# Optimization experiments

Measured on AMD Instinct MI355X. Metric: run time of the kernel, lower is better.

The kernel has to match this reference:

```python
import jax, jax.numpy as jnp
import numpy as np

POOL_LEN = 128  # agent tokens (AdaptiveAvgPool1d output size)

def setup_inputs() -> dict:
    key = jax.random.key(0)
    ks = jax.random.split(key, 7)
    B, D, L = 8, 512, 4096
    s = 1.0 / np.sqrt(D)
    return {
        "x":  jax.random.normal(ks[0], (B, D, L), dtype=jnp.float32),
        "Wq": jax.random.normal(ks[1], (D, D), dtype=jnp.float32) * s,
        "bq": jax.random.normal(ks[2], (D,), dtype=jnp.float32) * 0.01,
        "Wk": jax.random.normal(ks[3], (D, D), dtype=jnp.float32) * s,
        "bk": jax.random.normal(ks[4], (D,), dtype=jnp.float32) * 0.01,
        "Wv": jax.random.normal(ks[5], (D, D), dtype=jnp.float32) * s,
        "bv": jax.random.normal(ks[6], (D,), dtype=jnp.float32) * 0.01,
    }

def reference(x, Wq, bq, Wk, bk, Wv, bv):
    # x: [B, D, L] channel-first, as in the torch module
    xt = jnp.swapaxes(x, -1, -2)               # [B, L, D]
    q = xt @ Wq.T + bq                         # [B, L, D]
    k = xt @ Wk.T + bk                         # [B, L, D]
    v = xt @ Wv.T + bv                         # [B, L, D]
    B, L, D = q.shape
    # AdaptiveAvgPool1d(L -> POOL_LEN): uniform segment mean since L % POOL_LEN == 0
    a = q.reshape(B, POOL_LEN, L // POOL_LEN, D).mean(axis=2)  # [B, P, D]
    # stage 1: agents attend to keys, aggregate values (no 1/sqrt(d) scaling in original)
    c = jax.nn.softmax(jnp.einsum('bpd,bld->bpl', a, k), axis=-1) @ v  # [B, P, D]
    # stage 2: queries attend to agents
    r = jax.nn.softmax(jnp.einsum('bld,bpd->blp', q, a), axis=-1) @ c  # [B, L, D]
    return jnp.swapaxes(r, -1, -2)             # [B, D, L]
```

## Files before the change

### kernel.cpp

```cpp
#include <hip/hip_runtime.h>
#include <hip/hip_fp16.h>

typedef _Float16 f16;
using frag16 = __attribute__((ext_vector_type(8))) _Float16;
using f32x4  = __attribute__((ext_vector_type(4))) float;

__device__ __forceinline__ void gload_lds16(const void* g, void* l) {
    __builtin_amdgcn_global_load_lds(
        (const __attribute__((address_space(1))) void*)g,
        (__attribute__((address_space(3))) void*)l, 16, 0, 0);
}

__global__ __launch_bounds__(256) void cvt3_f16(const float* __restrict__ Wq,
                                                const float* __restrict__ Wk,
                                                const float* __restrict__ Wv,
                                                f16* __restrict__ out) {
    int i = blockIdx.x * 256 + threadIdx.x;
    const float* src = (i < 262144) ? Wq : (i < 524288) ? Wk : Wv;
    out[i] = (f16)src[i & 262143];
}

__global__ __launch_bounds__(256) void transpose_f32_f16(const float* __restrict__ in,
                                                         f16* __restrict__ out) {
    __shared__ float t[64][65];
    const int b = blockIdx.z;
    const int d0 = blockIdx.x * 64, l0 = blockIdx.y * 64;
    const float* ip = in + (size_t)b * 512 * 4096;
    f16* op = out + (size_t)b * 4096 * 512;
#pragma unroll
    for (int it = 0; it < 4; ++it) {
        int idx = it * 256 + threadIdx.x;
        int d = idx >> 4, c4 = (idx & 15) * 4;
        const float4 v = *reinterpret_cast<const float4*>(&ip[(size_t)(d0 + d) * 4096 + l0 + c4]);
        t[d][c4] = v.x; t[d][c4 + 1] = v.y; t[d][c4 + 2] = v.z; t[d][c4 + 3] = v.w;
    }
    __syncthreads();
#pragma unroll
    for (int it = 0; it < 2; ++it) {
        int idx = it * 256 + threadIdx.x;
        int l = idx >> 3, dg = (idx & 7) * 8;
        union { f16 h[8]; uint4 u; } pk;
#pragma unroll
        for (int k = 0; k < 8; ++k) pk.h[k] = (f16)t[dg + k][l];
        *reinterpret_cast<uint4*>(&op[(size_t)(l0 + l) * 512 + d0 + dg]) = pk.u;
    }
}

__global__ __launch_bounds__(256) void softmax4096(const float* __restrict__ S,
                                                   f16* __restrict__ P) {
    const float* s = S + (size_t)blockIdx.x * 4096;
    f16* p = P + (size_t)blockIdx.x * 4096;
    const int tid = threadIdx.x;
    float v[16];
    float mx = -3.0e38f;
#pragma unroll
    for (int i = 0; i < 16; ++i) { v[i] = s[i * 256 + tid]; mx = fmaxf(mx, v[i]); }
#pragma unroll
    for (int o = 32; o; o >>= 1) mx = fmaxf(mx, __shfl_xor(mx, o));
    __shared__ float redm[4];
    __shared__ float reds[4];
    if ((tid & 63) == 0) redm[tid >> 6] = mx;
    __syncthreads();
    mx = fmaxf(fmaxf(redm[0], redm[1]), fmaxf(redm[2], redm[3]));
    float sum = 0.f;
#pragma unroll
    for (int i = 0; i < 16; ++i) { v[i] = __expf(v[i] - mx); sum += v[i]; }
#pragma unroll
    for (int o = 32; o; o >>= 1) sum += __shfl_xor(sum, o);
    if ((tid & 63) == 0) reds[tid >> 6] = sum;
    __syncthreads();
    sum = reds[0] + reds[1] + reds[2] + reds[3];
    float inv = 1.f / sum;
#pragma unroll
    for (int i = 0; i < 16; ++i) p[i * 256 + tid] = (f16)(v[i] * inv);
}

__global__ __launch_bounds__(512) void gemm_qkv(
    const f16* __restrict__ xb, const f16* __restrict__ w,
    const float* __restrict__ bq, const float* __restrict__ bk,
    const float* __restrict__ bv,
    f16* __restrict__ qk, f16* __restrict__ vT, f16* __restrict__ a)
{
    __shared__ __align__(16) char smem[65536];
    const int tid = threadIdx.x;
    const int lane = tid & 63, wave = tid >> 6;
    const int wm = wave >> 2, wn = wave & 3;

    const int m0b = ((blockIdx.z << 3) + blockIdx.x) << 7;
    const int n0b = blockIdx.y << 7;

    const int lrow = lane & 15, kgrp = (lane >> 4) * 8;

    const int tr = tid >> 3;
    const int tcs = (((tid & 7) ^ (tr & 7)) * 8);
    const f16* gA = xb + (size_t)(m0b + tr) * 512 + tcs;
    const f16* gB = w  + (size_t)(n0b + tr) * 512 + tcs;

    f32x4 acc[4][2] = {};

    auto stage = [&](int bi, int k0) {
        char* sAp = smem + bi * 32768 + tid * 16;
        char* sBp = sAp + 16384;
        gload_lds16(gA + k0,                     sAp);
        gload_lds16(gA + (size_t)64 * 512 + k0,  sAp + 8192);
        gload_lds16(gB + k0,                     sBp);
        gload_lds16(gB + (size_t)64 * 512 + k0,  sBp + 8192);
    };
    auto compute = [&](int bi) {
        const char* base = smem + bi * 32768;
        const int swz = (lrow & 7) << 4;
        const int arow = wm * 64 + lrow;
        const int brow = wn * 32 + lrow;
#pragma unroll
        for (int kk = 0; kk < 2; ++kk) {
            const int colb = ((kgrp * 2) | (kk * 64)) ^ swz;
            frag16 af[4], bf[2];
#pragma unroll
            for (int i = 0; i < 4; ++i)
                af[i] = *(const frag16*)(base + (arow + i * 16) * 128 + colb);
#pragma unroll
            for (int j = 0; j < 2; ++j)
                bf[j] = *(const frag16*)(base + 16384 + (brow + j * 16) * 128 + colb);
#pragma unroll
            for (int i = 0; i < 4; ++i)
#pragma unroll
                for (int j = 0; j < 2; ++j)
                    acc[i][j] = __builtin_amdgcn_mfma_f32_16x16x32_f16(af[i], bf[j], acc[i][j], 0, 0, 0);
        }
    };

    stage(0, 0);
    int cur = 0;
#pragma unroll 1
    for (int t = 0; t < 7; ++t) {
        stage(cur ^ 1, (t + 1) * 64);
        asm volatile("s_waitcnt vmcnt(4)" ::: "memory");
        __builtin_amdgcn_s_barrier();
        __builtin_amdgcn_sched_barrier(0);
        compute(cur);
        __builtin_amdgcn_s_barrier();
        cur ^= 1;
    }
    asm volatile("s_waitcnt vmcnt(0)" ::: "memory");
    __builtin_amdgcn_s_barrier();
    __builtin_amdgcn_sched_barrier(0);
    compute(cur);
    __builtin_amdgcn_s_barrier();

    const int rbase = (lane >> 4) * 4;
    if (n0b < 1024) {
        const float* bptr = (n0b < 512) ? bq : bk;

        if (n0b < 512) {
            const int b = m0b >> 12;
            const int pbase = ((m0b & 4095) >> 5) + wm * 2;
#pragma unroll
            for (int j = 0; j < 2; ++j) {
                int d = n0b + wn * 32 + j * 16 + lrow;
                float badd = bptr[d];
                float s0 = 0.f, s1 = 0.f;
#pragma unroll
                for (int r = 0; r < 4; ++r) {
                    s0 += acc[0][j][r] + acc[1][j][r];
                    s1 += acc[2][j][r] + acc[3][j][r];
                }
                s0 += __shfl_xor(s0, 16); s0 += __shfl_xor(s0, 32);
                s1 += __shfl_xor(s1, 16); s1 += __shfl_xor(s1, 32);
                if (lane < 16) {
                    a[((size_t)(b * 128 + pbase)     * 512) + d] = (f16)(s0 * 0.03125f + badd);
                    a[((size_t)(b * 128 + pbase + 1) * 512) + d] = (f16)(s1 * 0.03125f + badd);
                }
            }
        }

        f16* lt = (f16*)smem;
#pragma unroll
        for (int j = 0; j < 2; ++j) {
            int col = wn * 32 + j * 16 + lrow;
            float badd = bptr[(n0b + col) & 511];
#pragma unroll
            for (int i = 0; i < 4; ++i) {
                int row = wm * 64 + i * 16 + rbase;
#pragma unroll
                for (int r = 0; r < 4; ++r)
                    lt[(row + r) * 136 + col] = (f16)(acc[i][j][r] + badd);
            }
        }
        __syncthreads();
#pragma unroll
        for (int it = 0; it < 4; ++it) {
            int cu = it * 512 + tid;
            int row = cu >> 4, c8 = (cu & 15) * 8;
            *reinterpret_cast<uint4*>(&qk[(size_t)(m0b + row) * 1024 + n0b + c8]) =
                *reinterpret_cast<const uint4*>(&lt[row * 136 + c8]);
        }
    } else {
        const int b = m0b >> 12, l0 = m0b & 4095;
        const int d0 = n0b - 1024;
        f16* vout = vT + (size_t)b * 2097152 + l0;
        float* lt = (float*)smem;
#pragma unroll
        for (int h = 0; h < 2; ++h) {
            if ((wn >> 1) == h) {
#pragma unroll
                for (int i = 0; i < 4; ++i)
#pragma unroll
                    for (int j = 0; j < 2; ++j)
#pragma unroll
                        for (int r = 0; r < 4; ++r)
                            lt[((wn & 1) * 32 + j * 16 + lrow) * 132 + wm * 64 + i * 16 + rbase + r]
                                = acc[i][j][r];
            }
            __syncthreads();
#pragma unroll
            for (int it = 0; it < 2; ++it) {
                int idx = it * 512 + tid;
                int nl = idx >> 4, mg = (idx & 15) * 8;
                int d = d0 + h * 64 + nl;
                float badd = bv[d];
                union { f16 hh[8]; uint4 u; } pk;
#pragma unroll
                for (int k = 0; k < 8; ++k)
                    pk.hh[k] = (f16)(lt[nl * 132 + mg + k] + badd);
                *reinterpret_cast<uint4*>(&vout[(size_t)d * 4096 + mg]) = pk.u;
            }
            __syncthreads();
        }
    }
}

template<bool OUT_F16, bool BIAS, bool TRANS_OUT>
__global__ __launch_bounds__(256) void gemm_lds(
    const f16* __restrict__ A, const f16* __restrict__ B,
    const float* __restrict__ bias, void* __restrict__ C,
    int K, int lda, int ldb, int ldc,
    long long sA, long long sB, long long sC, int splitk)
{
    __shared__ __align__(16) char smem[65536];
    const int z = blockIdx.z;
    const int batch = z / splitk;
    const int ks = z - batch * splitk;
    const int Ksub = K / splitk;
    const int kbeg = ks * Ksub;

    const f16* Ab = A + (size_t)batch * sA;
    const f16* Bb = B + (size_t)batch * sB;

    const int tid = threadIdx.x;
    const int lane = tid & 63, wave = tid >> 6;
    const int wm = wave >> 1, wn = wave & 1;
    const int m0b = blockIdx.x * 128, n0b = blockIdx.y * 128;
    const int lrow = lane & 15, kgrp = (lane >> 4) * 8;

    const int tr = tid >> 3;
    const int tcs = (((tid & 7) ^ (tr & 7)) * 8);
    const f16* gA = Ab + (size_t)(m0b + tr) * lda + tcs;
    const f16* gB = Bb + (size_t)(n0b + tr) * ldb + tcs;

    f32x4 acc[4][4] = {};

    auto stage = [&](int bi, int k0) {
        char* sAp = smem + bi * 32768 + tid * 16;
        char* sBp = sAp + 16384;
#pragma unroll
        for (int i = 0; i < 4; ++i) {
            gload_lds16(gA + (size_t)(i * 32) * lda + k0, sAp + i * 4096);
            gload_lds16(gB + (size_t)(i * 32) * ldb + k0, sBp + i * 4096);
        }
    };
    auto compute = [&](int bi) {
        const char* base = smem + bi * 32768;
        const int swz = (lrow & 7) << 4;
        const int arow = wm * 64 + lrow;
        const int brow = wn * 64 + lrow;
#pragma unroll
        for (int kk = 0; kk < 2; ++kk) {
            const int colb = ((kgrp * 2) | (kk * 64)) ^ swz;
            frag16 af[4], bf[4];
#pragma unroll
            for (int i = 0; i < 4; ++i)
                af[i] = *(const frag16*)(base + (arow + i * 16) * 128 + colb);
#pragma unroll
            for (int j = 0; j < 4; ++j)
                bf[j] = *(const frag16*)(base + 16384 + (brow + j * 16) * 128 + colb);
#pragma unroll
            for (int i = 0; i < 4; ++i)
#pragma unroll
                for (int j = 0; j < 4; ++j)
                    acc[i][j] = __builtin_amdgcn_mfma_f32_16x16x32_f16(af[i], bf[j], acc[i][j], 0, 0, 0);
        }
    };

    stage(0, kbeg);
    int cur = 0;
    const int nt = Ksub >> 6;
#pragma unroll 1
    for (int t = 0; t < nt - 1; ++t) {
        stage(cur ^ 1, kbeg + (t + 1) * 64);
        asm volatile("s_waitcnt vmcnt(8)" ::: "memory");
        __builtin_amdgcn_s_barrier();
        __builtin_amdgcn_sched_barrier(0);
        compute(cur);
        __builtin_amdgcn_s_barrier();
        cur ^= 1;
    }
    asm volatile("s_waitcnt vmcnt(0)" ::: "memory");
    __builtin_amdgcn_s_barrier();
    __builtin_amdgcn_sched_barrier(0);
    compute(cur);
    __builtin_amdgcn_s_barrier();

    const int rbase = (lane >> 4) * 4;
    const size_t cb = (size_t)z * sC;
    if constexpr (TRANS_OUT) {
        float* lt = (float*)smem;
#pragma unroll
        for (int h = 0; h < 2; ++h) {
            if (wn == h) {
#pragma unroll
                for (int i = 0; i < 4; ++i)
#pragma unroll
                    for (int j = 0; j < 4; ++j)
#pragma unroll
                        for (int r = 0; r < 4; ++r)
                            lt[(j * 16 + lrow) * 132 + wm * 64 + i * 16 + rbase + r] = acc[i][j][r];
            }
            __syncthreads();
#pragma unroll
            for (int it = 0; it < 32; ++it) {
                int idx = it * 256 + tid;
                int nl = idx >> 7, ml = idx & 127;
                int n = n0b + h * 64 + nl;
                float val = lt[nl * 132 + ml] + (BIAS ? bias[n] : 0.f);
                size_t o = cb + (size_t)n * ldc + m0b + ml;
                if constexpr (OUT_F16) ((f16*)C)[o] = (f16)val;
                else                   ((float*)C)[o] = val;
            }
            __syncthreads();
        }
    } else {
#pragma unroll
        for (int j = 0; j < 4; ++j) {
            int col = n0b + wn * 64 + j * 16 + lrow;
            float badd = BIAS ? bias[col] : 0.f;
#pragma unroll
            for (int i = 0; i < 4; ++i) {
                int row = m0b + wm * 64 + i * 16 + rbase;
#pragma unroll
                for (int r = 0; r < 4; ++r) {
                    float val = acc[i][j][r] + badd;
                    size_t o = cb + (size_t)(row + r) * ldc + col;
                    if constexpr (OUT_F16) ((f16*)C)[o] = (f16)val;
                    else                   ((float*)C)[o] = val;
                }
            }
        }
    }
}

__global__ __launch_bounds__(256) void reduce_pv(const float* __restrict__ Pp,
                                                 f16* __restrict__ cT) {
    int idx = blockIdx.x * 256 + threadIdx.x;
    int d = idx & 511, p = (idx >> 9) & 127, b = idx >> 16;
    float s = 0.f;
#pragma unroll
    for (int k = 0; k < 8; ++k)
        s += Pp[(size_t)(b * 8 + k) * 65536 + p * 512 + d];
    cT[(size_t)b * 65536 + d * 128 + p] = (f16)s;
}

__global__ __launch_bounds__(256) void attn2(
    const f16* __restrict__ qk, const f16* __restrict__ ab,
    const f16* __restrict__ cT, float* __restrict__ out)
{
    __shared__ __align__(16) char smem[69632];
    float* scr = (float*)(smem + 33280);
    f16*   P2  = (f16*)(smem + 34816);

    const int tid = threadIdx.x;
    const int lane = tid & 63, wave = tid >> 6;
    const int wm = wave >> 1, wn = wave & 1;
    const int l0 = blockIdx.x * 128;
    const int b  = blockIdx.y;
    const int lrow = lane & 15, kgrp = (lane >> 4) * 8, rbase = (lane >> 4) * 4;
    const int tr = tid >> 3, tc = (tid & 7) * 8;

    char* sAp = smem + tid * 16;
    char* sBp = smem + 16384 + tid * 16;

    const f16* gA = qk + (size_t)b * 4194304 + (size_t)(l0 + tr) * 1024 + tc;
    const f16* gB = ab + (size_t)b * 65536  + (size_t)tr * 512 + tc;

    f32x4 acc[4][4] = {};
#pragma unroll 1
    for (int k0 = 0; k0 < 512; k0 += 64) {
#pragma unroll
        for (int i = 0; i < 4; ++i) {
            gload_lds16(gA + (size_t)(i * 32) * 1024 + k0, sAp + i * 4096);
            gload_lds16(gB + (size_t)(i * 32) * 512  + k0, sBp + i * 4096);
        }
        __syncthreads();
        const f16* la = (const f16*)smem + (wm * 64 + lrow) * 64 + kgrp;
        const f16* lb = (const f16*)(smem + 16384) + (wn * 64 + lrow) * 64 + kgrp;
#pragma unroll
        for (int kk = 0; kk < 2; ++kk) {
            frag16 af[4], bf[4];
#pragma unroll
            for (int i = 0; i < 4; ++i) af[i] = *(const frag16*)(la + i * 16 * 64 + kk * 32);
#pragma unroll
            for (int j = 0; j < 4; ++j) bf[j] = *(const frag16*)(lb + j * 16 * 64 + kk * 32);
#pragma unroll
            for (int i = 0; i < 4; ++i)
#pragma unroll
                for (int j = 0; j < 4; ++j)
                    acc[i][j] = __builtin_amdgcn_mfma_f32_16x16x32_f16(af[i], bf[j], acc[i][j], 0, 0, 0);
        }
        __syncthreads();
    }

    float mx[4][4];
#pragma unroll
    for (int i = 0; i < 4; ++i)
#pragma unroll
        for (int r = 0; r < 4; ++r) {
            float m = fmaxf(fmaxf(acc[i][0][r], acc[i][1][r]),
                            fmaxf(acc[i][2][r], acc[i][3][r]));
            m = fmaxf(m, __shfl_xor(m, 1));
            m = fmaxf(m, __shfl_xor(m, 2));
            m = fmaxf(m, __shfl_xor(m, 4));
            m = fmaxf(m, __shfl_xor(m, 8));
            mx[i][r] = m;
        }
    if ((lane & 15) == 0) {
#pragma unroll
        for (int i = 0; i < 4; ++i)
#pragma unroll
            for (int r = 0; r < 4; ++r)
                scr[wn * 128 + wm * 64 + i * 16 + rbase + r] = mx[i][r];
    }
    __syncthreads();
    float rowm[4][4];
#pragma unroll
    for (int i = 0; i < 4; ++i)
#pragma unroll
        for (int r = 0; r < 4; ++r) {
            int row = wm * 64 + i * 16 + rbase + r;
            rowm[i][r] = fmaxf(scr[row], scr[128 + row]);
        }
    __syncthreads();
    float sum[4][4];
#pragma unroll
    for (int i = 0; i < 4; ++i)
#pragma unroll
        for (int r = 0; r < 4; ++r) {
            float s = 0.f;
#pragma unroll
            for (int j = 0; j < 4; ++j) {
                float p = __expf(acc[i][j][r] - rowm[i][r]);
                acc[i][j][r] = p;
                s += p;
            }
            s += __shfl_xor(s, 1);
            s += __shfl_xor(s, 2);
            s += __shfl_xor(s, 4);
            s += __shfl_xor(s, 8);
            sum[i][r] = s;
        }
    if ((lane & 15) == 0) {
#pragma unroll
        for (int i = 0; i < 4; ++i)
#pragma unroll
            for (int r = 0; r < 4; ++r)
                scr[wn * 128 + wm * 64 + i * 16 + rbase + r] = sum[i][r];
    }
    __syncthreads();
#pragma unroll
    for (int i = 0; i < 4; ++i)
#pragma unroll
        for (int r = 0; r < 4; ++r) {
            int row = wm * 64 + i * 16 + rbase + r;
            float inv = 1.f / (scr[row] + scr[128 + row]);
#pragma unroll
            for (int j = 0; j < 4; ++j)
                P2[row * 136 + wn * 64 + j * 16 + lrow] = (f16)(acc[i][j][r] * inv);
        }
    __syncthreads();

    const f16* gC = cT + (size_t)b * 65536;
    float* outb = out + (size_t)b * 512 * 4096;
#pragma unroll 1
    for (int c = 0; c < 4; ++c) {
        const int d0 = c * 128;
#pragma unroll
        for (int i = 0; i < 4; ++i) {
            gload_lds16(gC + (size_t)(d0 + tr + i * 32) * 128 + tc,      sAp + i * 4096);
            gload_lds16(gC + (size_t)(d0 + tr + i * 32) * 128 + tc + 64, sBp + i * 4096);
        }
        __syncthreads();
        f32x4 a2[4][4] = {};
#pragma unroll
        for (int half = 0; half < 2; ++half) {
            const f16* lb = (const f16*)(smem + half * 16384) + (wn * 64 + lrow) * 64 + kgrp;
            const f16* lpa = P2 + (wm * 64 + lrow) * 136 + half * 64 + kgrp;
#pragma unroll
            for (int kk = 0; kk < 2; ++kk) {
                frag16 af[4], bf[4];
#pragma unroll
                for (int i = 0; i < 4; ++i) af[i] = *(const frag16*)(lpa + i * 16 * 136 + kk * 32);
#pragma unroll
                for (int j = 0; j < 4; ++j) bf[j] = *(const frag16*)(lb + j * 16 * 64 + kk * 32);
#pragma unroll
                for (int i = 0; i < 4; ++i)
#pragma unroll
                    for (int j = 0; j < 4; ++j)
                        a2[i][j] = __builtin_amdgcn_mfma_f32_16x16x32_f16(af[i], bf[j], a2[i][j], 0, 0, 0);
            }
        }
        __syncthreads();

        float* lt = (float*)smem;
#pragma unroll
        for (int h = 0; h < 2; ++h) {
            if (wn == h) {
#pragma unroll
                for (int i = 0; i < 4; ++i)
#pragma unroll
                    for (int j = 0; j < 4; ++j)
#pragma unroll
                        for (int r = 0; r < 4; ++r)
                            lt[(j * 16 + lrow) * 132 + wm * 64 + i * 16 + rbase + r] = a2[i][j][r];
            }
            __syncthreads();
#pragma unroll
            for (int it = 0; it < 8; ++it) {
                int idx = it * 256 + tid;
                int nl = idx >> 5, mq = (idx & 31) * 4;
                float4 v = *reinterpret_cast<const float4*>(&lt[nl * 132 + mq]);
                *reinterpret_cast<float4*>(&outb[(size_t)(d0 + h * 64 + nl) * 4096 + l0 + mq]) = v;
            }
            __syncthreads();
        }
    }
}

extern "C" void kernel_launch(void* const* d_in, const int* in_sizes, int n_in,
                              void* d_out, int out_size, void* d_ws, size_t ws_size,
                              hipStream_t stream) {
    const float* x  = (const float*)d_in[0];
    const float* Wq = (const float*)d_in[1];
    const float* bq = (const float*)d_in[2];
    const float* Wk = (const float*)d_in[3];
    const float* bk = (const float*)d_in[4];
    const float* Wv = (const float*)d_in[5];
    const float* bv = (const float*)d_in[6];
    float* out = (float*)d_out;

    const size_t o_xb = 0;
    const size_t o_qk = 33554432;
    const size_t o_vT = 100663296;
    const size_t o_w  = 134217728;
    const size_t o_ab = o_w + 1572864;
    const size_t o_cT = o_ab + 1048576;
    const size_t o_S  = o_cT + 1048576;
    const size_t o_P  = o_S + 16777216;
    const size_t need = o_P + 8388608;
    if (ws_size < need) return;

    char* ws = (char*)d_ws;
    f16* xb   = (f16*)(ws + o_xb);
    f16* qk   = (f16*)(ws + o_qk);
    f16* vT   = (f16*)(ws + o_vT);
    f16* wqkv = (f16*)(ws + o_w);
    f16* ab   = (f16*)(ws + o_ab);
    f16* cT   = (f16*)(ws + o_cT);
    float* Sb = (float*)(ws + o_S);
    float* Pp = (float*)(ws + o_S);
    f16* Pb   = (f16*)(ws + o_P);

    cvt3_f16<<<3072, 256, 0, stream>>>(Wq, Wk, Wv, wqkv);

    transpose_f32_f16<<<dim3(8, 64, 8), 256, 0, stream>>>(x, xb);

    gemm_qkv<<<dim3(8, 12, 32), 512, 0, stream>>>(xb, wqkv, bq, bk, bv, qk, vT, ab);

    gemm_lds<false, false, false><<<dim3(1, 32, 8), 256, 0, stream>>>(
        ab, qk + 512, nullptr, Sb, 512, 512, 1024, 4096, 65536LL, 4194304LL, 524288LL, 1);

    softmax4096<<<1024, 256, 0, stream>>>(Sb, Pb);

    gemm_lds<false, false, false><<<dim3(1, 4, 64), 256, 0, stream>>>(
        Pb, vT, nullptr, Pp, 4096, 4096, 4096, 512, 524288LL, 2097152LL, 65536LL, 8);
    reduce_pv<<<2048, 256, 0, stream>>>(Pp, cT);

    attn2<<<dim3(32, 8), 256, 0, stream>>>(qk, ab, cT, out);
}
```

Before: 160.0 us.

## Store scores and split-K partials in fp16, widen gemm to 8 waves

The score matrix and the split-K partial products are now written and read as fp16 instead of fp32, which halves the intermediate memory traffic. The softmax and reduce kernels switch to vectorized 16-byte loads and stores. The generic LDS GEMM moves to 512 threads with 8 waves, each computing a 64x32 sub-tile, so each thread issues fewer loads and more waves are in flight. Split-K for the PV product goes from 8 to 16, giving more blocks but more partials to reduce. The risk is precision: unscaled logits stored in fp16 may lose accuracy or overflow, and fp16 partials may round before summation.

Result: no change. 160.3 us (+0.2%).

```diff
diff --git a/kernel.cpp b/kernel.cpp
--- a/kernel.cpp
+++ b/kernel.cpp
@@ -46,15 +46,18 @@
     }
 }
 
-__global__ __launch_bounds__(256) void softmax4096(const float* __restrict__ S,
+__global__ __launch_bounds__(256) void softmax4096(const f16* __restrict__ S,
                                                    f16* __restrict__ P) {
-    const float* s = S + (size_t)blockIdx.x * 4096;
+    const f16* s = S + (size_t)blockIdx.x * 4096;
     f16* p = P + (size_t)blockIdx.x * 4096;
     const int tid = threadIdx.x;
-    float v[16];
+    union { f16 h[16]; uint4 u[2]; } v;
+    v.u[0] = *reinterpret_cast<const uint4*>(&s[tid * 16]);
+    v.u[1] = *reinterpret_cast<const uint4*>(&s[tid * 16 + 8]);
+    float f[16];
     float mx = -3.0e38f;
 #pragma unroll
-    for (int i = 0; i < 16; ++i) { v[i] = s[i * 256 + tid]; mx = fmaxf(mx, v[i]); }
+    for (int i = 0; i < 16; ++i) { f[i] = (float)v.h[i]; mx = fmaxf(mx, f[i]); }
 #pragma unroll
     for (int o = 32; o; o >>= 1) mx = fmaxf(mx, __shfl_xor(mx, o));
     __shared__ float redm[4];
@@ -64,7 +67,7 @@
     mx = fmaxf(fmaxf(redm[0], redm[1]), fmaxf(redm[2], redm[3]));
     float sum = 0.f;
 #pragma unroll
-    for (int i = 0; i < 16; ++i) { v[i] = __expf(v[i] - mx); sum += v[i]; }
+    for (int i = 0; i < 16; ++i) { f[i] = __expf(f[i] - mx); sum += f[i]; }
 #pragma unroll
     for (int o = 32; o; o >>= 1) sum += __shfl_xor(sum, o);
     if ((tid & 63) == 0) reds[tid >> 6] = sum;
@@ -72,7 +75,9 @@
     sum = reds[0] + reds[1] + reds[2] + reds[3];
     float inv = 1.f / sum;
 #pragma unroll
-    for (int i = 0; i < 16; ++i) p[i * 256 + tid] = (f16)(v[i] * inv);
+    for (int i = 0; i < 16; ++i) v.h[i] = (f16)(f[i] * inv);
+    *reinterpret_cast<uint4*>(&p[tid * 16])     = v.u[0];
+    *reinterpret_cast<uint4*>(&p[tid * 16 + 8]) = v.u[1];
 }
 
 __global__ __launch_bounds__(512) void gemm_qkv(
@@ -229,10 +234,10 @@
     }
 }
 
-template<bool OUT_F16, bool BIAS, bool TRANS_OUT>
-__global__ __launch_bounds__(256) void gemm_lds(
+template<bool OUT_F16>
+__global__ __launch_bounds__(512) void gemm_lds(
     const f16* __restrict__ A, const f16* __restrict__ B,
-    const float* __restrict__ bias, void* __restrict__ C,
+    void* __restrict__ C,
     int K, int lda, int ldb, int ldc,
     long long sA, long long sB, long long sC, int splitk)
 {
@@ -248,7 +253,7 @@
 
     const int tid = threadIdx.x;
     const int lane = tid & 63, wave = tid >> 6;
-    const int wm = wave >> 1, wn = wave & 1;
+    const int wm = wave >> 2, wn = wave & 3;
     const int m0b = blockIdx.x * 128, n0b = blockIdx.y * 128;
     const int lrow = lane & 15, kgrp = (lane >> 4) * 8;
 
@@ -257,36 +262,35 @@
     const f16* gA = Ab + (size_t)(m0b + tr) * lda + tcs;
     const f16* gB = Bb + (size_t)(n0b + tr) * ldb + tcs;
 
-    f32x4 acc[4][4] = {};
+    f32x4 acc[4][2] = {};
 
     auto stage = [&](int bi, int k0) {
         char* sAp = smem + bi * 32768 + tid * 16;
         char* sBp = sAp + 16384;
-#pragma unroll
-        for (int i = 0; i < 4; ++i) {
-            gload_lds16(gA + (size_t)(i * 32) * lda + k0, sAp + i * 4096);
-            gload_lds16(gB + (size_t)(i * 32) * ldb + k0, sBp + i * 4096);
-        }
+        gload_lds16(gA + k0,                     sAp);
+        gload_lds16(gA + (size_t)64 * lda + k0,  sAp + 8192);
+        gload_lds16(gB + k0,                     sBp);
+        gload_lds16(gB + (size_t)64 * ldb + k0,  sBp + 8192);
     };
     auto compute = [&](int bi) {
         const char* base = smem + bi * 32768;
         const int swz = (lrow & 7) << 4;
         const int arow = wm * 64 + lrow;
-        const int brow = wn * 64 + lrow;
+        const int brow = wn * 32 + lrow;
 #pragma unroll
         for (int kk = 0; kk < 2; ++kk) {
             const int colb = ((kgrp * 2) | (kk * 64)) ^ swz;
-            frag16 af[4], bf[4];
+            frag16 af[4], bf[2];
 #pragma unroll
             for (int i = 0; i < 4; ++i)
                 af[i] = *(const frag16*)(base + (arow + i * 16) * 128 + colb);
 #pragma unroll
-            for (int j = 0; j < 4; ++j)
+            for (int j = 0; j < 2; ++j)
                 bf[j] = *(const frag16*)(base + 16384 + (brow + j * 16) * 128 + colb);
 #pragma unroll
             for (int i = 0; i < 4; ++i)
 #pragma unroll
-                for (int j = 0; j < 4; ++j)
+                for (int j = 0; j < 2; ++j)
                     acc[i][j] = __builtin_amdgcn_mfma_f32_16x16x32_f16(af[i], bf[j], acc[i][j], 0, 0, 0);
         }
     };
@@ -297,7 +301,7 @@
 #pragma unroll 1
     for (int t = 0; t < nt - 1; ++t) {
         stage(cur ^ 1, kbeg + (t + 1) * 64);
-        asm volatile("s_waitcnt vmcnt(8)" ::: "memory");
+        asm volatile("s_waitcnt vmcnt(4)" ::: "memory");
         __builtin_amdgcn_s_barrier();
         __builtin_amdgcn_sched_barrier(0);
         compute(cur);
@@ -312,61 +316,39 @@
 
     const int rbase = (lane >> 4) * 4;
     const size_t cb = (size_t)z * sC;
-    if constexpr (TRANS_OUT) {
-        float* lt = (float*)smem;
-#pragma unroll
-        for (int h = 0; h < 2; ++h) {
-            if (wn == h) {
-#pragma unroll
-                for (int i = 0; i < 4; ++i)
-#pragma unroll
-                    for (int j = 0; j < 4; ++j)
-#pragma unroll
-                        for (int r = 0; r < 4; ++r)
-                            lt[(j * 16 + lrow) * 132 + wm * 64 + i * 16 + rbase + r] = acc[i][j][r];
-            }
-            __syncthreads();
-#pragma unroll
-            for (int it = 0; it < 32; ++it) {
-                int idx = it * 256 + tid;
-                int nl = idx >> 7, ml = idx & 127;
-                int n = n0b + h * 64 + nl;
-                float val = lt[nl * 132 + ml] + (BIAS ? bias[n] : 0.f);
-                size_t o = cb + (size_t)n * ldc + m0b + ml;
+#pragma unroll
+    for (int j = 0; j < 2; ++j) {
+        int col = n0b + wn * 32 + j * 16 + lrow;
+#pragma unroll
+        for (int i = 0; i < 4; ++i) {
+            int row = m0b + wm * 64 + i * 16 + rbase;
+#pragma unroll
+            for (int r = 0; r < 4; ++r) {
+                float val = acc[i][j][r];
+                size_t o = cb + (size_t)(row + r) * ldc + col;
                 if constexpr (OUT_F16) ((f16*)C)[o] = (f16)val;
                 else                   ((float*)C)[o] = val;
             }
-            __syncthreads();
-        }
-    } else {
-#pragma unroll
-        for (int j = 0; j < 4; ++j) {
-            int col = n0b + wn * 64 + j * 16 + lrow;
-            float badd = BIAS ? bias[col] : 0.f;
-#pragma unroll
-            for (int i = 0; i < 4; ++i) {
-                int row = m0b + wm * 64 + i * 16 + rbase;
-#pragma unroll
-                for (int r = 0; r < 4; ++r) {
-                    float val = acc[i][j][r] + badd;
-                    size_t o = cb + (size_t)(row + r) * ldc + col;
-                    if constexpr (OUT_F16) ((f16*)C)[o] = (f16)val;
-                    else                   ((float*)C)[o] = val;
-                }
-            }
-        }
-    }
-}
-
-__global__ __launch_bounds__(256) void reduce_pv(const float* __restrict__ Pp,
+        }
+    }
+}
+
+__global__ __launch_bounds__(256) void reduce_pv(const f16* __restrict__ Pp,
                                                  f16* __restrict__ cT) {
     int idx = blockIdx.x * 256 + threadIdx.x;
-    int d = idx & 511, p = (idx >> 9) & 127, b = idx >> 16;
-    float s = 0.f;
-#pragma unroll
-    for (int k = 0; k < 8; ++k)
-        s += Pp[(size_t)(b * 8 + k) * 65536 + p * 512 + d];
-    cT[(size_t)b * 65536 + d * 128 + p] = (f16)s;
+    int dg = (idx & 63) * 8, p = (idx >> 6) & 127, b = idx >> 13;
+    float s[8] = {};
+#pragma unroll
+    for (int k = 0; k < 16; ++k) {
+        union { uint4 u; f16 h[8]; } v;
+        v.u = *reinterpret_cast<const uint4*>(
+            &Pp[(size_t)(b * 16 + k) * 65536 + p * 512 + dg]);
+#pragma unroll
+        for (int e = 0; e < 8; ++e) s[e] += (float)v.h[e];
+    }
+#pragma unroll
+    for (int e = 0; e < 8; ++e)
+        cT[(size_t)b * 65536 + (size_t)(dg + e) * 128 + p] = (f16)s[e];
 }
 
 __global__ __launch_bounds__(256) void attn2(
@@ -573,8 +555,8 @@
     f16* wqkv = (f16*)(ws + o_w);
     f16* ab   = (f16*)(ws + o_ab);
     f16* cT   = (f16*)(ws + o_cT);
-    float* Sb = (float*)(ws + o_S);
-    float* Pp = (float*)(ws + o_S);
+    f16* Sb   = (f16*)(ws + o_S);
+    f16* Pp   = (f16*)(ws + o_S);
     f16* Pb   = (f16*)(ws + o_P);
 
     cvt3_f16<<<3072, 256, 0, stream>>>(Wq, Wk, Wv, wqkv);
@@ -583,14 +565,14 @@
 
     gemm_qkv<<<dim3(8, 12, 32), 512, 0, stream>>>(xb, wqkv, bq, bk, bv, qk, vT, ab);
 
-    gemm_lds<false, false, false><<<dim3(1, 32, 8), 256, 0, stream>>>(
-        ab, qk + 512, nullptr, Sb, 512, 512, 1024, 4096, 65536LL, 4194304LL, 524288LL, 1);
+    gemm_lds<true><<<dim3(1, 32, 8), 512, 0, stream>>>(
+        ab, qk + 512, Sb, 512, 512, 1024, 4096, 65536LL, 4194304LL, 524288LL, 1);
 
     softmax4096<<<1024, 256, 0, stream>>>(Sb, Pb);
 
-    gemm_lds<false, false, false><<<dim3(1, 4, 64), 256, 0, stream>>>(
-        Pb, vT, nullptr, Pp, 4096, 4096, 4096, 512, 524288LL, 2097152LL, 65536LL, 8);
-    reduce_pv<<<2048, 256, 0, stream>>>(Pp, cT);
+    gemm_lds<true><<<dim3(1, 4, 128), 512, 0, stream>>>(
+        Pb, vT, Pp, 4096, 4096, 4096, 512, 524288LL, 2097152LL, 65536LL, 16);
+    reduce_pv<<<256, 256, 0, stream>>>(Pp, cT);
 
     attn2<<<dim3(32, 8), 256, 0, stream>>>(qk, ab, cT, out);
 }
```
